# Optimization experiments

Measured on AMD Instinct MI355X. Metric: run time of the kernel, lower is better.

Reference implementation:

```python
import jax, jax.numpy as jnp
import numpy as np

N_NODES = 50000
N_EDGES = 1_600_000
F_IN = 32
HIDDEN = 32
HORIZON = 12
K = 2


def setup_inputs() -> dict:
    key = jax.random.key(0)
    ks = jax.random.split(key, 12)
    s = 0.1  # keep gates away from saturation
    x = jax.random.normal(ks[0], (N_NODES, 1, F_IN), dtype=jnp.float32)
    edge_index = jax.random.randint(ks[1], (2, N_EDGES), 0, N_NODES, dtype=jnp.int64)
    edge_weight = jax.random.uniform(ks[2], (N_EDGES,), dtype=jnp.float32)
    Wx = jax.random.normal(ks[3], (4, K, F_IN, HIDDEN), dtype=jnp.float32) * s
    bx = jax.random.normal(ks[4], (4, HIDDEN), dtype=jnp.float32) * s
    Wh = jax.random.normal(ks[5], (4, K, HIDDEN, HIDDEN), dtype=jnp.float32) * s
    bh = jax.random.normal(ks[6], (4, HIDDEN), dtype=jnp.float32) * s
    wc = jax.random.normal(ks[7], (3, HIDDEN), dtype=jnp.float32) * s
    b = jax.random.normal(ks[8], (4, HIDDEN), dtype=jnp.float32) * s
    W_lin = jax.random.normal(ks[9], (HIDDEN, HORIZON), dtype=jnp.float32) * s
    b_lin = jax.random.normal(ks[10], (HORIZON,), dtype=jnp.float32) * s
    h0 = jnp.zeros((N_NODES, HIDDEN), dtype=jnp.float32)
    c0 = jnp.zeros((N_NODES, HIDDEN), dtype=jnp.float32)
    return dict(x=x, edge_index=edge_index, edge_weight=edge_weight, Wx=Wx, bx=bx,
                Wh=Wh, bh=bh, wc=wc, b=b, W_lin=W_lin, b_lin=b_lin, h0=h0, c0=c0)


def reference(x, edge_index, edge_weight, Wx, bx, Wh, bh, wc, b, W_lin, b_lin, h0, c0):
    N = x.shape[0]
    src, dst = edge_index[0], edge_index[1]
    # ChebConv sym normalization with lambda_max=2: L_hat = L - I = -D^{-1/2} A D^{-1/2}
    deg = jax.ops.segment_sum(edge_weight, src, num_segments=N)
    dinv = jnp.where(deg > 0, jax.lax.rsqrt(deg), 0.0)
    nw = -dinv[src] * edge_weight * dinv[dst]  # [E]

    X = x[:, 0, :]  # squeeze(1) -> [N, F]

    def cheb(Z, W, bb):
        # K=2 Chebyshev: T0(Z)=Z, T1(Z)=L_hat Z (sparse gather-scatter)
        LZ = jax.ops.segment_sum(nw[:, None] * Z[src], dst, num_segments=N)
        return Z @ W[0] + LZ @ W[1] + bb

    # gate order: i, f, c, o
    I = jax.nn.sigmoid(cheb(X, Wx[0], bx[0]) + cheb(h0, Wh[0], bh[0]) + wc[0] * c0 + b[0])
    Fg = jax.nn.sigmoid(cheb(X, Wx[1], bx[1]) + cheb(h0, Wh[1], bh[1]) + wc[1] * c0 + b[1])
    T = jnp.tanh(cheb(X, Wx[2], bx[2]) + cheb(h0, Wh[2], bh[2]) + b[2])
    C = Fg * c0 + I * T
    O = jax.nn.sigmoid(cheb(X, Wx[3], bx[3]) + cheb(h0, Wh[3], bh[3]) + wc[2] * C + b[3])
    H = O * jnp.tanh(C)

    h = jax.nn.relu(H) @ W_lin + b_lin  # Linear(32, horizon)
    return (h, H, C)
```

## Files before the change

kernel.cpp:

```cpp
#include <hip/hip_runtime.h>
#include <math.h>

#define HID 32
#define HOR 12
#define NB  256
#define GSH 8
#define GW  256
#define NPT 4

__device__ __forceinline__ float sigmoidf_(float x) { return 1.0f / (1.0f + expf(-x)); }


__global__ __launch_bounds__(1024) void k_hist(const int* __restrict__ src,
                                               const int* __restrict__ dst,
                                               int* __restrict__ hist,
                                               int E, int chunk, int ng) {
    __shared__ int hS[GW], hD[GW];
    int t = threadIdx.x, b = blockIdx.x;
    for (int i = t; i < ng; i += 1024) { hS[i] = 0; hD[i] = 0; }
    __syncthreads();
    int beg = b * chunk, end = min(E, beg + chunk);
    for (int e = beg + t; e < end; e += 1024) {
        atomicAdd(&hS[src[e] >> GSH], 1);
        atomicAdd(&hD[dst[e] >> GSH], 1);
    }
    __syncthreads();
    for (int i = t; i < ng; i += 1024) {
        hist[(size_t)i * NB + b] = hS[i];
        hist[((size_t)ng + i) * NB + b] = hD[i];
    }
}

__global__ __launch_bounds__(256) void k_binscan(const int* __restrict__ hist,
                                                 int* __restrict__ off,
                                                 int* __restrict__ binTot, int ng2) {
    __shared__ int s[256];
    int b2 = blockIdx.x, t = threadIdx.x;
    int v = hist[(size_t)b2 * NB + t];
    s[t] = v;
    __syncthreads();
    for (int o = 1; o < 256; o <<= 1) {
        int x = (t >= o) ? s[t - o] : 0;
        __syncthreads();
        s[t] += x;
        __syncthreads();
    }
    off[(size_t)t * ng2 + b2] = s[t] - v;
    if (t == 255) binTot[b2] = s[255];
}

__global__ __launch_bounds__(1024) void k_binbase(const int* __restrict__ binTot,
                                                  int* __restrict__ baseS, int* __restrict__ baseD,
                                                  int* __restrict__ rowptr,
                                                  int E, int ng, int N) {
    __shared__ int buf[1024];
    int t = threadIdx.x;
    int isD = blockIdx.x;
    int sum = (t < ng) ? binTot[isD * ng + t] : 0;
    buf[t] = sum;
    __syncthreads();
    for (int o = 1; o < 1024; o <<= 1) {
        int v = (t >= o) ? buf[t - o] : 0;
        __syncthreads();
        buf[t] += v;
        __syncthreads();
    }
    int base = buf[t] - sum;
    int* B = isD ? baseD : baseS;
    if (t < ng) B[t] = base;
    if (t == 0) { B[ng] = E; if (!isD) rowptr[N] = E; }
}

__global__ __launch_bounds__(1024) void k_scatter(const int* __restrict__ src,
                                                  const int* __restrict__ dst,
                                                  const float* __restrict__ w,
                                                  const int* __restrict__ off,
                                                  const int* __restrict__ baseS,
                                                  const int* __restrict__ baseD,
                                                  int2* __restrict__ tmpS, int2* __restrict__ tmpD,
                                                  int E, int chunk, int ng) {
    __shared__ int cS[GW], cD[GW];
    int t = threadIdx.x, b = blockIdx.x;
    int ng2 = 2 * ng;
    for (int i = t; i < ng; i += 1024) {
        cS[i] = off[(size_t)b * ng2 + i] + baseS[i];
        cD[i] = off[(size_t)b * ng2 + ng + i] + baseD[i];
    }
    __syncthreads();
    int beg = b * chunk, end = min(E, beg + chunk);
    for (int e = beg + t; e < end; e += 1024) {
        int s = src[e], d = dst[e];
        int wb = __float_as_int(w[e]);
        int pS = atomicAdd(&cS[s >> GSH], 1);
        tmpS[pS] = make_int2(s, wb);
        int pD = atomicAdd(&cD[d >> GSH], 1);
        tmpD[pD] = make_int2(s | ((d & (GW - 1)) << 16), wb);
    }
}

__global__ __launch_bounds__(256) void k_degsum(const int2* __restrict__ tmpS,
                                                const int* __restrict__ baseS,
                                                float* __restrict__ dinv, int N) {
    __shared__ float h[GW];
    int g = blockIdx.x, t = threadIdx.x;
    h[t] = 0.0f;
    __syncthreads();
    int beg = baseS[g], end = baseS[g + 1];
    for (int i = beg + t; i < end; i += 256) {
        int2 p = tmpS[i];
        atomicAdd(&h[p.x & (GW - 1)], __int_as_float(p.y));
    }
    __syncthreads();
    int n = (g << GSH) + t;
    if (n < N) { float s = h[t]; dinv[n] = (s > 0.0f) ? rsqrtf(s) : 0.0f; }
}

__global__ __launch_bounds__(256) void k_scatter2(const int2* __restrict__ tmpD,
                                                  const int* __restrict__ baseD,
                                                  const float* __restrict__ dinv,
                                                  int* __restrict__ rowptr,
                                                  int2* __restrict__ epair, int N) {
    __shared__ int h[GW], cur[GW];
    int g = blockIdx.x, t = threadIdx.x;
    h[t] = 0;
    __syncthreads();
    int beg = baseD[g], end = baseD[g + 1];
    for (int i = beg + t; i < end; i += 256) atomicAdd(&h[(tmpD[i].x >> 16) & (GW - 1)], 1);
    __syncthreads();
    int v = h[t];
    for (int o = 1; o < GW; o <<= 1) {
        int x = (t >= o) ? h[t - o] : 0;
        __syncthreads();
        h[t] += x;
        __syncthreads();
    }
    int excl = h[t] - v;
    int n = (g << GSH) + t;
    if (n < N) rowptr[n] = beg + excl;
    cur[t] = beg + excl;
    __syncthreads();
    for (int i = beg + t; i < end; i += 256) {
        int2 p = tmpD[i];
        int low = (p.x >> 16) & (GW - 1);
        int s = p.x & 0xFFFF;
        int pos = atomicAdd(&cur[low], 1);
        float nw = -dinv[s] * __int_as_float(p.y) * dinv[(g << GSH) + low];
        epair[pos] = make_int2(s, __float_as_int(nw));
    }
}

__global__ void k_flags(const float* __restrict__ h0, const float* __restrict__ c0,
                        int* __restrict__ flag, int total) {
    int i = blockIdx.x * 256 + threadIdx.x;
    float a = (i < total) ? h0[i] : 0.0f;
    float c = (i < total) ? c0[i] : 0.0f;
    unsigned long long ba = __ballot(a != 0.0f);
    unsigned long long bc = __ballot(c != 0.0f);
    if ((threadIdx.x & 63) == 0) {
        int m = (ba ? 1 : 0) | (bc ? 2 : 0);
        if (m) atomicOr(flag, m);
    }
}

__global__ __launch_bounds__(256) void k_gather(const int* __restrict__ rowptr,
                                                const int2* __restrict__ epair,
                                                const float* __restrict__ X,
                                                const float* __restrict__ H0,
                                                const int* __restrict__ hflag,
                                                float* __restrict__ LX, float* __restrict__ LH,
                                                int N) {
    int tid = blockIdx.x * 256 + threadIdx.x;
    int n = tid >> 5;
    int f = tid & 31;
    if (n >= N) return;
    int beg = rowptr[n], end = rowptr[n + 1];
    float acc = 0.0f, accH = 0.0f;
    int fl = *hflag;
    if (fl & 1) {
        #pragma unroll 4
        for (int i = beg; i < end; ++i) {
            int2 p = epair[i];
            float w = __int_as_float(p.y);
            acc  += w * X[(p.x << 5) + f];
            accH += w * H0[(p.x << 5) + f];
        }
    } else {
        #pragma unroll 4
        for (int i = beg; i < end; ++i) {
            int2 p = epair[i];
            acc += __int_as_float(p.y) * X[(p.x << 5) + f];
        }
    }
    LX[(n << 5) + f] = acc;
    if (fl & 1) LH[(n << 5) + f] = accH;
}

__global__ __launch_bounds__(256) void k_gates(
    const float* __restrict__ X, const float* __restrict__ LX,
    const float* __restrict__ H0, const float* __restrict__ LH,
    const float* __restrict__ C0,
    const float* __restrict__ Wx, const float* __restrict__ bx,
    const float* __restrict__ Wh, const float* __restrict__ bh,
    const float* __restrict__ wc, const float* __restrict__ b,
    const float* __restrict__ Wl, const float* __restrict__ bl,
    const int* __restrict__ flag,
    float* __restrict__ hOut, float* __restrict__ outH, float* __restrict__ outC,
    int N) {
    int tid = blockIdx.x * 256 + threadIdx.x;
    int g = tid >> 5;
    int j = tid & 31;
    int n0 = g * NPT;
    if (n0 >= N) return;
    int cnt = min(NPT, N - n0);
    int f2 = *flag;
    float blv = (j < HOR) ? bl[j] : 0.0f;

    if (f2 == 0) {
        float xk[NPT], lxk[NPT];
        #pragma unroll
        for (int i = 0; i < NPT; ++i) { xk[i] = 0.0f; lxk[i] = 0.0f; }
        for (int i = 0; i < cnt; ++i) {
            int base = (n0 + i) << 5;
            xk[i]  = X[base + j];
            lxk[i] = LX[base + j];
        }
        float p0[NPT], p2[NPT], p3[NPT];
        float b0 = bx[0 * HID + j] + bh[0 * HID + j] + b[0 * HID + j];
        float b2 = bx[2 * HID + j] + bh[2 * HID + j] + b[2 * HID + j];
        float b3 = bx[3 * HID + j] + bh[3 * HID + j] + b[3 * HID + j];
        #pragma unroll
        for (int i = 0; i < NPT; ++i) { p0[i] = b0; p2[i] = b2; p3[i] = b3; }

        #pragma unroll 4
        for (int k = 0; k < HID; ++k) {
            int row = k * HID + j;
            float w00 = Wx[0 * 2048 + row], w01 = Wx[0 * 2048 + 1024 + row];
            float w20 = Wx[2 * 2048 + row], w21 = Wx[2 * 2048 + 1024 + row];
            float w30 = Wx[3 * 2048 + row], w31 = Wx[3 * 2048 + 1024 + row];
            #pragma unroll
            for (int i = 0; i < NPT; ++i) {
                float xv  = __shfl(xk[i],  k, 32);
                float lxv = __shfl(lxk[i], k, 32);
                p0[i] += xv * w00 + lxv * w01;
                p2[i] += xv * w20 + lxv * w21;
                p3[i] += xv * w30 + lxv * w31;
            }
        }

        float wc2 = wc[2 * HID + j];
        for (int i = 0; i < cnt; ++i) {
            int n = n0 + i;
            int base = n << 5;
            float I = sigmoidf_(p0[i]);
            float T = tanhf(p2[i]);
            float C = I * T;
            float O = sigmoidf_(p3[i] + wc2 * C);
            float H = O * tanhf(C);
            outH[base + j] = H;
            outC[base + j] = C;
            float ah = blv;
            #pragma unroll 8
            for (int k = 0; k < HID; ++k) {
                float hv = __shfl(H, k, 32);
                if (j < HOR) ah += fmaxf(hv, 0.0f) * Wl[k * HOR + j];
            }
            if (j < HOR) hOut[n * HOR + j] = ah;
        }
        return;
    }

    float xk[NPT], lxk[NPT], hk[NPT], lhk[NPT];
    #pragma unroll
    for (int i = 0; i < NPT; ++i) { xk[i] = 0.0f; lxk[i] = 0.0f; hk[i] = 0.0f; lhk[i] = 0.0f; }
    for (int i = 0; i < cnt; ++i) {
        int base = (n0 + i) << 5;
        xk[i]  = X[base + j];
        lxk[i] = LX[base + j];
        hk[i]  = H0[base + j];
        lhk[i] = (f2 & 1) ? LH[base + j] : 0.0f;
    }

    float pre[4][NPT];
    #pragma unroll
    for (int gt = 0; gt < 4; ++gt) {
        float bb = bx[gt * HID + j] + bh[gt * HID + j] + b[gt * HID + j];
        #pragma unroll
        for (int i = 0; i < NPT; ++i) pre[gt][i] = bb;
    }

    #pragma unroll 2
    for (int k = 0; k < HID; ++k) {
        float w0[4], w1[4], w2[4], w3[4];
        int row = k * HID + j;
        #pragma unroll
        for (int gt = 0; gt < 4; ++gt) {
            w0[gt] = Wx[gt * 2048 + row];
            w1[gt] = Wx[gt * 2048 + 1024 + row];
            w2[gt] = Wh[gt * 2048 + row];
            w3[gt] = Wh[gt * 2048 + 1024 + row];
        }
        #pragma unroll
        for (int i = 0; i < NPT; ++i) {
            float xv  = __shfl(xk[i],  k, 32);
            float lxv = __shfl(lxk[i], k, 32);
            float hv  = __shfl(hk[i],  k, 32);
            float lhv = __shfl(lhk[i], k, 32);
            #pragma unroll
            for (int gt = 0; gt < 4; ++gt)
                pre[gt][i] += xv * w0[gt] + lxv * w1[gt] + hv * w2[gt] + lhv * w3[gt];
        }
    }

    float wc0 = wc[0 * HID + j], wc1 = wc[1 * HID + j], wc2 = wc[2 * HID + j];
    for (int i = 0; i < cnt; ++i) {
        int n = n0 + i;
        int base = n << 5;
        float c0v = C0[base + j];
        float I  = sigmoidf_(pre[0][i] + wc0 * c0v);
        float Fg = sigmoidf_(pre[1][i] + wc1 * c0v);
        float T  = tanhf(pre[2][i]);
        float C  = Fg * c0v + I * T;
        float O  = sigmoidf_(pre[3][i] + wc2 * C);
        float H  = O * tanhf(C);
        outH[base + j] = H;
        outC[base + j] = C;
        float ah = blv;
        #pragma unroll 8
        for (int k = 0; k < HID; ++k) {
            float hv = __shfl(H, k, 32);
            if (j < HOR) ah += fmaxf(hv, 0.0f) * Wl[k * HOR + j];
        }
        if (j < HOR) hOut[n * HOR + j] = ah;
    }
}

extern "C" void kernel_launch(void* const* d_in, const int* in_sizes, int n_in,
                              void* d_out, int out_size, void* d_ws, size_t ws_size,
                              hipStream_t stream) {
    const float* x  = (const float*)d_in[0];
    const int*   ei = (const int*)d_in[1];
    const float* ew = (const float*)d_in[2];
    const float* Wx = (const float*)d_in[3];
    const float* bx = (const float*)d_in[4];
    const float* Wh = (const float*)d_in[5];
    const float* bh = (const float*)d_in[6];
    const float* wc = (const float*)d_in[7];
    const float* b  = (const float*)d_in[8];
    const float* Wl = (const float*)d_in[9];
    const float* bl = (const float*)d_in[10];
    const float* h0 = (const float*)d_in[11];
    const float* c0 = (const float*)d_in[12];

    int N = in_sizes[0] / HID;
    int E = in_sizes[2];
    const int* src = ei;
    const int* dst = ei + E;

    int ng = (N + GW - 1) >> GSH;
    int ng2 = 2 * ng;
    int chunk = (E + NB - 1) / NB;

    int* wsi = (int*)d_ws;
    int2*  tmpD   = (int2*)wsi;
    int2*  tmpS   = (int2*)(wsi + 2 * (size_t)E);
    int2*  epair  = tmpS;
    float* LX     = (float*)(wsi + 4 * (size_t)E);
    float* LH     = LX + (size_t)N * HID;
    int*   rowptr = (int*)(LH + (size_t)N * HID);
    int*   hist   = rowptr + (N + 1);
    int*   off    = hist + (size_t)ng2 * NB;
    int*   binTot = off + (size_t)ng2 * NB;
    int*   baseS  = binTot + 2048;
    int*   baseD  = baseS + (ng + 1);
    float* dinv   = (float*)(baseD + (ng + 1));
    int*   flag   = (int*)(dinv + N);

    float* hOut = (float*)d_out;
    float* HOut = hOut + (size_t)N * HOR;
    float* COut = HOut + (size_t)N * HID;

    hipMemsetAsync(flag, 0, sizeof(int), stream);

    k_hist<<<NB, 1024, 0, stream>>>(src, dst, hist, E, chunk, ng);
    k_binscan<<<ng2, 256, 0, stream>>>(hist, off, binTot, ng2);
    k_binbase<<<2, 1024, 0, stream>>>(binTot, baseS, baseD, rowptr, E, ng, N);
    k_scatter<<<NB, 1024, 0, stream>>>(src, dst, ew, off, baseS, baseD, tmpS, tmpD, E, chunk, ng);
    k_degsum<<<ng, 256, 0, stream>>>(tmpS, baseS, dinv, N);
    k_flags<<<(N * HID + 255) / 256, 256, 0, stream>>>(h0, c0, flag, N * HID);
    k_scatter2<<<ng, 256, 0, stream>>>(tmpD, baseD, dinv, rowptr, epair, N);

    k_gather<<<(N * HID + 255) / 256, 256, 0, stream>>>(rowptr, epair, x, h0, flag, LX, LH, N);

    int gThreads = ((N + NPT - 1) / NPT) * 32;
    k_gates<<<(gThreads + 255) / 256, 256, 0, stream>>>(x, LX, h0, LH, c0,
                                                        Wx, bx, Wh, bh, wc, b, Wl, bl, flag,
                                                        hOut, HOut, COut, N);
}
```

Baseline: 274.8 us.

## Restructure zero-state gate kernel to node-per-lane with uniform weight loads

In the zero-state path of the gate kernel, each lane now owns one node and one wave owns a slice of eight hidden units. Inputs are loaded as float4 vectors and weight reads are wave-uniform, which replaces the per-k cross-lane shuffles of the old layout. The output linear layer goes through shared memory so that each wave computes three horizon outputs for 64 nodes, instead of leaving 20 of 32 lanes idle. The cost is higher register pressure from the per-lane 32-element arrays, and the fast path relies on the launch grid covering at least ceil(N/64) blocks.

```diff
diff --git a/kernel.cpp b/kernel.cpp
--- a/kernel.cpp
+++ b/kernel.cpp
@@ -206,68 +206,104 @@
     const int* __restrict__ flag,
     float* __restrict__ hOut, float* __restrict__ outH, float* __restrict__ outC,
     int N) {
+    __shared__ float Hl[HID][64];
+    int f2 = *flag;
+
+    if (f2 == 0) {
+        int fastB = (N + 63) >> 6;
+        if (blockIdx.x >= fastB) return;
+        int t = threadIdx.x;
+        int ln = t & 63;
+        int n = (blockIdx.x << 6) + ln;
+        int jc = __builtin_amdgcn_readfirstlane(t >> 6);
+        int j0 = jc << 3;
+
+        if (n < N) {
+            const float4* Xr = (const float4*)(X + ((size_t)n << 5));
+            const float4* Lr = (const float4*)(LX + ((size_t)n << 5));
+            float4 x4[8], l4[8];
+            #pragma unroll
+            for (int q = 0; q < 8; ++q) { x4[q] = Xr[q]; l4[q] = Lr[q]; }
+            float xr[HID], lr[HID];
+            #pragma unroll
+            for (int q = 0; q < 8; ++q) {
+                xr[4*q+0] = x4[q].x; xr[4*q+1] = x4[q].y; xr[4*q+2] = x4[q].z; xr[4*q+3] = x4[q].w;
+                lr[4*q+0] = l4[q].x; lr[4*q+1] = l4[q].y; lr[4*q+2] = l4[q].z; lr[4*q+3] = l4[q].w;
+            }
+
+            float aI[8], aT[8], aO[8];
+            #pragma unroll
+            for (int jj = 0; jj < 8; ++jj) {
+                aI[jj] = bx[j0 + jj]           + bh[j0 + jj]           + b[j0 + jj];
+                aT[jj] = bx[2*HID + j0 + jj]   + bh[2*HID + j0 + jj]   + b[2*HID + j0 + jj];
+                aO[jj] = bx[3*HID + j0 + jj]   + bh[3*HID + j0 + jj]   + b[3*HID + j0 + jj];
+            }
+
+            const float* W0x = Wx + j0;
+            const float* W0l = Wx + 1024 + j0;
+            const float* W2x = Wx + 2*2048 + j0;
+            const float* W2l = Wx + 2*2048 + 1024 + j0;
+            const float* W3x = Wx + 3*2048 + j0;
+            const float* W3l = Wx + 3*2048 + 1024 + j0;
+
+            #pragma unroll
+            for (int k = 0; k < HID; ++k) {
+                float xv = xr[k], lv = lr[k];
+                int r = k << 5;
+                #pragma unroll
+                for (int jj = 0; jj < 8; ++jj) {
+                    aI[jj] += xv * W0x[r + jj] + lv * W0l[r + jj];
+                    aT[jj] += xv * W2x[r + jj] + lv * W2l[r + jj];
+                    aO[jj] += xv * W3x[r + jj] + lv * W3l[r + jj];
+                }
+            }
+
+            float h8[8], c8[8];
+            #pragma unroll
+            for (int jj = 0; jj < 8; ++jj) {
+                float I = sigmoidf_(aI[jj]);
+                float T = tanhf(aT[jj]);
+                float C = I * T;
+                float O = sigmoidf_(aO[jj] + wc[2*HID + j0 + jj] * C);
+                float H = O * tanhf(C);
+                h8[jj] = H;
+                c8[jj] = C;
+                Hl[j0 + jj][ln] = fmaxf(H, 0.0f);
+            }
+            size_t base = ((size_t)n << 5) + j0;
+            *(float4*)(outH + base)     = make_float4(h8[0], h8[1], h8[2], h8[3]);
+            *(float4*)(outH + base + 4) = make_float4(h8[4], h8[5], h8[6], h8[7]);
+            *(float4*)(outC + base)     = make_float4(c8[0], c8[1], c8[2], c8[3]);
+            *(float4*)(outC + base + 4) = make_float4(c8[4], c8[5], c8[6], c8[7]);
+        }
+        __syncthreads();
+
+        int hn = t & 63;
+        int hw = __builtin_amdgcn_readfirstlane(t >> 6);
+        int n2 = (blockIdx.x << 6) + hn;
+        if (n2 < N) {
+            int jb = hw * 3;
+            float a0 = bl[jb], a1 = bl[jb + 1], a2 = bl[jb + 2];
+            #pragma unroll
+            for (int k = 0; k < HID; ++k) {
+                float hv = Hl[k][hn];
+                a0 += hv * Wl[k * HOR + jb];
+                a1 += hv * Wl[k * HOR + jb + 1];
+                a2 += hv * Wl[k * HOR + jb + 2];
+            }
+            size_t ob = (size_t)n2 * HOR + jb;
+            hOut[ob] = a0; hOut[ob + 1] = a1; hOut[ob + 2] = a2;
+        }
+        return;
+    }
+
     int tid = blockIdx.x * 256 + threadIdx.x;
     int g = tid >> 5;
     int j = tid & 31;
     int n0 = g * NPT;
     if (n0 >= N) return;
     int cnt = min(NPT, N - n0);
-    int f2 = *flag;
     float blv = (j < HOR) ? bl[j] : 0.0f;
-
-    if (f2 == 0) {
-        float xk[NPT], lxk[NPT];
-        #pragma unroll
-        for (int i = 0; i < NPT; ++i) { xk[i] = 0.0f; lxk[i] = 0.0f; }
-        for (int i = 0; i < cnt; ++i) {
-            int base = (n0 + i) << 5;
-            xk[i]  = X[base + j];
-            lxk[i] = LX[base + j];
-        }
-        float p0[NPT], p2[NPT], p3[NPT];
-        float b0 = bx[0 * HID + j] + bh[0 * HID + j] + b[0 * HID + j];
-        float b2 = bx[2 * HID + j] + bh[2 * HID + j] + b[2 * HID + j];
-        float b3 = bx[3 * HID + j] + bh[3 * HID + j] + b[3 * HID + j];
-        #pragma unroll
-        for (int i = 0; i < NPT; ++i) { p0[i] = b0; p2[i] = b2; p3[i] = b3; }
-
-        #pragma unroll 4
-        for (int k = 0; k < HID; ++k) {
-            int row = k * HID + j;
-            float w00 = Wx[0 * 2048 + row], w01 = Wx[0 * 2048 + 1024 + row];
-            float w20 = Wx[2 * 2048 + row], w21 = Wx[2 * 2048 + 1024 + row];
-            float w30 = Wx[3 * 2048 + row], w31 = Wx[3 * 2048 + 1024 + row];
-            #pragma unroll
-            for (int i = 0; i < NPT; ++i) {
-                float xv  = __shfl(xk[i],  k, 32);
-                float lxv = __shfl(lxk[i], k, 32);
-                p0[i] += xv * w00 + lxv * w01;
-                p2[i] += xv * w20 + lxv * w21;
-                p3[i] += xv * w30 + lxv * w31;
-            }
-        }
-
-        float wc2 = wc[2 * HID + j];
-        for (int i = 0; i < cnt; ++i) {
-            int n = n0 + i;
-            int base = n << 5;
-            float I = sigmoidf_(p0[i]);
-            float T = tanhf(p2[i]);
-            float C = I * T;
-            float O = sigmoidf_(p3[i] + wc2 * C);
-            float H = O * tanhf(C);
-            outH[base + j] = H;
-            outC[base + j] = C;
-            float ah = blv;
-            #pragma unroll 8
-            for (int k = 0; k < HID; ++k) {
-                float hv = __shfl(H, k, 32);
-                if (j < HOR) ah += fmaxf(hv, 0.0f) * Wl[k * HOR + j];
-            }
-            if (j < HOR) hOut[n * HOR + j] = ah;
-        }
-        return;
-    }
 
     float xk[NPT], lxk[NPT], hk[NPT], lhk[NPT];
     #pragma unroll
@@ -330,7 +366,7 @@
             float hv = __shfl(H, k, 32);
             if (j < HOR) ah += fmaxf(hv, 0.0f) * Wl[k * HOR + j];
         }
-        if (j < HOR) hOut[n * HOR + j] = ah;
+        if (j < HOR) hOut[(size_t)n * HOR + j] = ah;
     }
 }
 
```

Measured after the change: 376.4 us. 1.37x slower.
